# Optimization experiments

Hardware: AMD Instinct MI355X
Metric: run time of the kernel (lower is better)

Reference implementation:

```python
import jax, jax.numpy as jnp
import numpy as np

N_NODES = 10000
N_EDGES = 80000
IN_DIM = 1024
HID = 4096
OUT = 256


def sage_conv(x, src, dst, W_l, b_l, W_r, num_nodes):
    # mean aggregation of source-node features onto target nodes
    msg = x[src]                                            # [E, D] gather
    agg = jax.ops.segment_sum(msg, dst, num_segments=num_nodes)   # [N, D]
    cnt = jax.ops.segment_sum(jnp.ones((src.shape[0],), x.dtype), dst,
                              num_segments=num_nodes)       # [N]
    mean = agg / jnp.clip(cnt, 1.0)[:, None]                # isolated nodes -> 0
    # lin_l(mean) + lin_r(x); lin_r has no bias in PyG SAGEConv
    return mean @ W_l.T + b_l + x @ W_r.T


def setup_inputs() -> dict:
    key = jax.random.key(0)
    ks = jax.random.split(key, 6)
    x = jax.random.normal(ks[0], (N_NODES, IN_DIM), dtype=jnp.float32)
    edge_index = jax.random.randint(ks[1], (2, N_EDGES), 0, N_NODES, dtype=jnp.int32)
    s1 = 1.0 / np.sqrt(IN_DIM)
    s2 = 1.0 / np.sqrt(HID)
    W1_l = jax.random.normal(ks[2], (HID, IN_DIM), dtype=jnp.float32) * s1
    b1_l = jnp.zeros((HID,), jnp.float32)
    W1_r = jax.random.normal(ks[3], (HID, IN_DIM), dtype=jnp.float32) * s1
    W2_l = jax.random.normal(ks[4], (OUT, HID), dtype=jnp.float32) * s2
    b2_l = jnp.zeros((OUT,), jnp.float32)
    W2_r = jax.random.normal(ks[5], (OUT, HID), dtype=jnp.float32) * s2
    return {"x": x, "edge_index": edge_index, "W1_l": W1_l, "b1_l": b1_l,
            "W1_r": W1_r, "W2_l": W2_l, "b2_l": b2_l, "W2_r": W2_r}


def reference(x, edge_index, W1_l, b1_l, W1_r, W2_l, b2_l, W2_r):
    src, dst = edge_index[0], edge_index[1]
    h = sage_conv(x, src, dst, W1_l, b1_l, W1_r, N_NODES)   # [N, 4096]
    h = jax.nn.relu(h)
    # dropout is identity in eval mode
    out = sage_conv(h, src, dst, W2_l, b2_l, W2_r, N_NODES)  # [N, 256]
    return jax.nn.log_softmax(out, axis=1)
```

## Files before the change

### kernel.cpp

```cpp
#include <hip/hip_runtime.h>
#include <cstdint>
#include <cstddef>

#define DEVINL __device__ __forceinline__

typedef __bf16 bf16x8 __attribute__((ext_vector_type(8)));
typedef float f32x4 __attribute__((ext_vector_type(4)));

static constexpr int NN = 10000;
static constexpr int NE = 80000;
static constexpr int IN_DIM = 1024;
static constexpr int HID = 4096;
static constexpr int OUTD = 256;
static constexpr int M_PAD = 10112;

DEVINL unsigned short f2bf(float f) {
  unsigned int u = __builtin_bit_cast(unsigned int, f);
  u += 0x7fffu + ((u >> 16) & 1u);
  return (unsigned short)(u >> 16);
}

DEVINL void ld_lds16(const void* g, void* l) {
  __builtin_amdgcn_global_load_lds(
      (const __attribute__((address_space(1))) unsigned int*)g,
      (__attribute__((address_space(3))) unsigned int*)l, 16, 0, 0);
}

__global__ void deg_kernel(const int* __restrict__ dst, int* __restrict__ deg) {
  int e = blockIdx.x * 256 + threadIdx.x;
  if (e < NE) atomicAdd(&deg[dst[e]], 1);
}

__global__ __launch_bounds__(256) void scan_kernel(const int* __restrict__ deg,
                                                   int* __restrict__ offs) {
  __shared__ int part[256];
  constexpr int NPT = 40;
  int t = threadIdx.x;
  int base = t * NPT;
  int s = 0;
  for (int j = 0; j < NPT; ++j) {
    int n = base + j;
    s += (n < NN) ? deg[n] : 0;
  }
  part[t] = s;
  __syncthreads();
  for (int o = 1; o < 256; o <<= 1) {
    int v = (t >= o) ? part[t - o] : 0;
    __syncthreads();
    part[t] += v;
    __syncthreads();
  }
  int pre = (t > 0) ? part[t - 1] : 0;
  for (int j = 0; j < NPT; ++j) {
    int n = base + j;
    if (n < NN) {
      offs[n] = pre;
      pre += deg[n];
    }
  }
  if (t == 255) offs[NN] = part[255];
}

__global__ void bin_kernel(const int* __restrict__ src, const int* __restrict__ dst,
                           const int* __restrict__ offs, int* __restrict__ fill,
                           int* __restrict__ csr) {
  int e = blockIdx.x * 256 + threadIdx.x;
  if (e < NE) {
    int d = dst[e];
    int p = atomicAdd(&fill[d], 1);
    csr[offs[d] + p] = src[e];
  }
}

__global__ __launch_bounds__(256) void gather1_kernel(const float* __restrict__ x,
                                                      const int* __restrict__ offs,
                                                      const int* __restrict__ csr,
                                                      unsigned short* __restrict__ A1) {
  int i = blockIdx.x;
  int t = threadIdx.x;
  int beg = offs[i], end = offs[i + 1];
  float4 acc = {0.f, 0.f, 0.f, 0.f};
  for (int j = beg; j < end; ++j) {
    int s = __builtin_amdgcn_readfirstlane(csr[j]);
    float4 v = ((const float4*)(x + (size_t)s * IN_DIM))[t];
    acc.x += v.x; acc.y += v.y; acc.z += v.z; acc.w += v.w;
  }
  float inv = 1.0f / (float)max(end - beg, 1);
  float4 b = ((const float4*)(x + (size_t)i * IN_DIM))[t];
  ushort4 pa = {f2bf(acc.x * inv), f2bf(acc.y * inv), f2bf(acc.z * inv), f2bf(acc.w * inv)};
  ushort4 pb = {f2bf(b.x), f2bf(b.y), f2bf(b.z), f2bf(b.w)};
  unsigned short* row = A1 + (size_t)i * 2048;
  ((ushort4*)row)[t] = pa;
  ((ushort4*)(row + 1024))[t] = pb;
}

__global__ void conv_w1_kernel(const float* __restrict__ Wl, const float* __restrict__ Wr,
                               unsigned short* __restrict__ w1cat) {
  int g = blockIdx.x * 256 + threadIdx.x;
  int n = g >> 9;
  int kg = g & 511;
  const float* s = (kg < 256) ? (Wl + (size_t)n * 1024 + kg * 4)
                              : (Wr + (size_t)n * 1024 + (kg - 256) * 4);
  float4 v = *(const float4*)s;
  ushort4 p = {f2bf(v.x), f2bf(v.y), f2bf(v.z), f2bf(v.w)};
  ((ushort4*)w1cat)[g] = p;
}

__global__ void conv_w2_kernel(const float* __restrict__ Wl, const float* __restrict__ Wr,
                               unsigned short* __restrict__ w2cat) {
  int g = blockIdx.x * 256 + threadIdx.x;
  int n = g >> 10;
  int kg = g & 1023;
  const float* s = (n < 256) ? (Wl + (size_t)n * 4096 + kg * 4)
                             : (Wr + (size_t)(n - 256) * 4096 + kg * 4);
  float4 v = *(const float4*)s;
  ushort4 p = {f2bf(v.x), f2bf(v.y), f2bf(v.z), f2bf(v.w)};
  ((ushort4*)w2cat)[g] = p;
}

template <int BM, int K, int N, int NUMM, int NUMN, int GM, bool EPI_RELU_BF16>
__global__ __launch_bounds__(256) void gemm_kernel(const unsigned short* __restrict__ A,
                                                   const unsigned short* __restrict__ Bt,
                                                   const float* __restrict__ bias,
                                                   void* __restrict__ Cout) {
  constexpr int BN = 128;
  constexpr int MI = BM / 32;
  constexpr int NI = 4;
  constexpr int SA = BM / 64;
  constexpr int SB = BN / 64;
  __shared__ unsigned short Asm[BM * 32];
  __shared__ unsigned short Bsm[BN * 32];

  constexpr int NPG = GM * NUMN;
  const int pid = blockIdx.x;
  const int gid = pid / NPG;
  const int first_m = gid * GM;
  const int sz = (NUMM - first_m < GM) ? (NUMM - first_m) : GM;
  const int local = pid % NPG;
  const int pm = first_m + local % sz;
  const int pn = local / sz;

  const int tid = threadIdx.x;
  const int lane = tid & 63;
  const int wave = tid >> 6;
  const int quad = lane >> 4;
  const int l16 = lane & 15;
  const int wm = (wave & 1) * (BM / 2);
  const int wn = (wave >> 1) * 64;
  const long tm0 = (long)pm * BM;
  const long tn0 = (long)pn * BN;

  f32x4 acc[MI][NI];
#pragma unroll
  for (int i = 0; i < MI; ++i)
#pragma unroll
    for (int j = 0; j < NI; ++j) acc[i][j] = (f32x4){0.f, 0.f, 0.f, 0.f};

  const unsigned short* aSrc[SA];
  unsigned short* aDst[SA];
  const unsigned short* bSrc[SB];
  unsigned short* bDst[SB];
#pragma unroll
  for (int s = 0; s < SA; ++s) {
    int c = s * 256 + wave * 64 + lane;
    int r = c >> 2;
    int g = (c & 3) ^ ((r >> 1) & 3);
    aSrc[s] = A + (size_t)(tm0 + r) * K + g * 8;
    aDst[s] = Asm + s * 2048 + wave * 512;
  }
#pragma unroll
  for (int s = 0; s < SB; ++s) {
    int c = s * 256 + wave * 64 + lane;
    int r = c >> 2;
    int g = (c & 3) ^ ((r >> 1) & 3);
    bSrc[s] = Bt + (size_t)(tn0 + r) * K + g * 8;
    bDst[s] = Bsm + s * 2048 + wave * 512;
  }

  const int srd = quad ^ ((l16 >> 1) & 3);

  for (int k0 = 0; k0 < K; k0 += 32) {
#pragma unroll
    for (int s = 0; s < SA; ++s) ld_lds16(aSrc[s] + k0, aDst[s]);
#pragma unroll
    for (int s = 0; s < SB; ++s) ld_lds16(bSrc[s] + k0, bDst[s]);
    __syncthreads();

    bf16x8 af[MI], bv[NI];
#pragma unroll
    for (int i = 0; i < MI; ++i) {
      int ra = wm + i * 16 + l16;
      af[i] = *(const bf16x8*)(Asm + ra * 32 + srd * 8);
    }
#pragma unroll
    for (int j = 0; j < NI; ++j) {
      int rb = wn + j * 16 + l16;
      bv[j] = *(const bf16x8*)(Bsm + rb * 32 + srd * 8);
    }
#pragma unroll
    for (int i = 0; i < MI; ++i)
#pragma unroll
      for (int j = 0; j < NI; ++j)
        acc[i][j] = __builtin_amdgcn_mfma_f32_16x16x32_bf16(af[i], bv[j], acc[i][j], 0, 0, 0);
    __syncthreads();
  }

  if (EPI_RELU_BF16) {
    unsigned short* C = (unsigned short*)Cout;
#pragma unroll
    for (int i = 0; i < MI; ++i) {
      long m0 = tm0 + wm + i * 16 + quad * 4;
#pragma unroll
      for (int j = 0; j < NI; ++j) {
        int n = (int)tn0 + wn + j * 16 + l16;
        float bvs = bias[n];
#pragma unroll
        for (int r = 0; r < 4; ++r) {
          float v = acc[i][j][r] + bvs;
          v = fmaxf(v, 0.0f);
          C[(size_t)(m0 + r) * N + n] = f2bf(v);
        }
      }
    }
  } else {
    float* C = (float*)Cout;
#pragma unroll
    for (int i = 0; i < MI; ++i) {
      long m0 = tm0 + wm + i * 16 + quad * 4;
#pragma unroll
      for (int j = 0; j < NI; ++j) {
        int n = (int)tn0 + wn + j * 16 + l16;
#pragma unroll
        for (int r = 0; r < 4; ++r) C[(size_t)(m0 + r) * N + n] = acc[i][j][r];
      }
    }
  }
}

__global__ __launch_bounds__(256) void gather2_final_kernel(const float* __restrict__ C2,
                                                            const int* __restrict__ offs,
                                                            const int* __restrict__ csr,
                                                            const float* __restrict__ b2,
                                                            float* __restrict__ out) {
  int i = blockIdx.x;
  int t = threadIdx.x;
  int beg = offs[i], end = offs[i + 1];
  float acc = 0.f;
  for (int j = beg; j < end; ++j) {
    int s = __builtin_amdgcn_readfirstlane(csr[j]);
    acc += C2[(size_t)s * 512 + t];
  }
  float inv = 1.0f / (float)max(end - beg, 1);
  float v = acc * inv + b2[t] + C2[(size_t)i * 512 + 256 + t];

  __shared__ float sm[4], ss[4];
  int w = t >> 6;
  float m = v;
#pragma unroll
  for (int o = 32; o > 0; o >>= 1) m = fmaxf(m, __shfl_xor(m, o, 64));
  if ((t & 63) == 0) sm[w] = m;
  __syncthreads();
  m = fmaxf(fmaxf(sm[0], sm[1]), fmaxf(sm[2], sm[3]));

  float e = __expf(v - m);
  float s = e;
#pragma unroll
  for (int o = 32; o > 0; o >>= 1) s += __shfl_xor(s, o, 64);
  if ((t & 63) == 0) ss[w] = s;
  __syncthreads();
  s = ss[0] + ss[1] + ss[2] + ss[3];

  out[(size_t)i * OUTD + t] = v - m - logf(s);
}

static constexpr size_t OFF_A1 = 0;
static constexpr size_t OFF_W1 = OFF_A1 + (size_t)M_PAD * 2048 * 2;
static constexpr size_t OFF_HB = OFF_W1 + (size_t)HID * 2048 * 2;
static constexpr size_t OFF_W2 = OFF_HB + (size_t)M_PAD * HID * 2;
static constexpr size_t OFF_DEG = OFF_W2 + (size_t)512 * HID * 2;
static constexpr size_t OFF_OFFS = OFF_DEG + (size_t)NN * 4;
static constexpr size_t OFF_FILL = OFF_OFFS + (size_t)(NN + 4) * 4;
static constexpr size_t OFF_CSR = OFF_FILL + (size_t)NN * 4;

extern "C" void kernel_launch(void* const* d_in, const int* in_sizes, int n_in,
                              void* d_out, int out_size, void* d_ws, size_t ws_size,
                              hipStream_t stream) {
  const float* x = (const float*)d_in[0];
  const int* ei = (const int*)d_in[1];
  const int* src = ei;
  const int* dst = ei + NE;
  const float* W1_l = (const float*)d_in[2];
  const float* b1_l = (const float*)d_in[3];
  const float* W1_r = (const float*)d_in[4];
  const float* W2_l = (const float*)d_in[5];
  const float* b2_l = (const float*)d_in[6];
  const float* W2_r = (const float*)d_in[7];
  float* out = (float*)d_out;

  char* ws = (char*)d_ws;
  unsigned short* A1 = (unsigned short*)(ws + OFF_A1);
  unsigned short* w1cat = (unsigned short*)(ws + OFF_W1);
  unsigned short* h_b = (unsigned short*)(ws + OFF_HB);
  unsigned short* w2cat = (unsigned short*)(ws + OFF_W2);
  int* deg = (int*)(ws + OFF_DEG);
  int* offs = (int*)(ws + OFF_OFFS);
  int* fill = (int*)(ws + OFF_FILL);
  int* csr = (int*)(ws + OFF_CSR);
  float* C2 = (float*)(ws + OFF_A1);

  hipMemsetAsync(deg, 0, (size_t)NN * 4, stream);
  hipMemsetAsync(fill, 0, (size_t)NN * 4, stream);
  hipMemsetAsync(A1 + (size_t)NN * 2048, 0, (size_t)(M_PAD - NN) * 2048 * 2, stream);

  deg_kernel<<<(NE + 255) / 256, 256, 0, stream>>>(dst, deg);
  scan_kernel<<<1, 256, 0, stream>>>(deg, offs);
  bin_kernel<<<(NE + 255) / 256, 256, 0, stream>>>(src, dst, offs, fill, csr);

  conv_w1_kernel<<<(HID * 512) / 256, 256, 0, stream>>>(W1_l, W1_r, w1cat);
  conv_w2_kernel<<<(512 * 1024) / 256, 256, 0, stream>>>(W2_l, W2_r, w2cat);

  gather1_kernel<<<NN, 256, 0, stream>>>(x, offs, csr, A1);

  gemm_kernel<128, 2048, 4096, 79, 32, 32, true>
      <<<79 * 32, 256, 0, stream>>>(A1, w1cat, b1_l, h_b);
  gemm_kernel<64, 4096, 512, 158, 4, 64, false>
      <<<158 * 4, 256, 0, stream>>>(h_b, w2cat, nullptr, C2);

  gather2_final_kernel<<<NN, 256, 0, stream>>>(C2, offs, csr, b2_l, out);
}
```

Baseline: 514.0 us.

## Gather from bf16 copies of x and layer-2 partials; fuse prep kernels

Converts x to bf16 once in a merged prep kernel that also handles both weight conversions and the degree count, so the layer-1 gather reads half the bytes per neighbour. The layer-2 GEMM now writes the neighbour-aggregated half as bf16 and the self half as fp32 in separate buffers, and the final gather/log-softmax uses 128 threads that each handle two outputs. This cuts gather memory traffic and launch count, at the cost of summing bf16-rounded values rather than fp32 ones.

```diff
diff --git a/kernel.cpp b/kernel.cpp
--- a/kernel.cpp
+++ b/kernel.cpp
@@ -19,6 +19,10 @@
   u += 0x7fffu + ((u >> 16) & 1u);
   return (unsigned short)(u >> 16);
 }
+DEVINL float bf2f(unsigned short h) {
+  unsigned int u = ((unsigned int)h) << 16;
+  return __builtin_bit_cast(float, u);
+}
 
 DEVINL void ld_lds16(const void* g, void* l) {
   __builtin_amdgcn_global_load_lds(
@@ -26,9 +30,48 @@
       (__attribute__((address_space(3))) unsigned int*)l, 16, 0, 0);
 }
 
-__global__ void deg_kernel(const int* __restrict__ dst, int* __restrict__ deg) {
-  int e = blockIdx.x * 256 + threadIdx.x;
-  if (e < NE) atomicAdd(&deg[dst[e]], 1);
+static constexpr int PREP_B1 = 8192;
+static constexpr int PREP_B2 = PREP_B1 + 2048;
+static constexpr int PREP_B3 = PREP_B2 + 10000;
+static constexpr int PREP_NB = PREP_B3 + 313;
+
+__global__ __launch_bounds__(256) void prep_kernel(
+    const float* __restrict__ W1l, const float* __restrict__ W1r,
+    const float* __restrict__ W2l, const float* __restrict__ W2r,
+    const float* __restrict__ x, const int* __restrict__ dst,
+    unsigned short* __restrict__ w1cat, unsigned short* __restrict__ w2cat,
+    unsigned short* __restrict__ x_bf, int* __restrict__ deg) {
+  int b = blockIdx.x;
+  int t = threadIdx.x;
+  if (b < PREP_B1) {
+    int g = b * 256 + t;
+    int n = g >> 9;
+    int kg = g & 511;
+    const float* s = (kg < 256) ? (W1l + (size_t)n * 1024 + kg * 4)
+                                : (W1r + (size_t)n * 1024 + (kg - 256) * 4);
+    float4 v = *(const float4*)s;
+    ushort4 p = {f2bf(v.x), f2bf(v.y), f2bf(v.z), f2bf(v.w)};
+    ((ushort4*)w1cat)[g] = p;
+  } else if (b < PREP_B2) {
+    int g = (b - PREP_B1) * 256 + t;
+    int n = g >> 10;
+    int kg = g & 1023;
+    const float* s = (n < 256) ? (W2l + (size_t)n * 4096 + kg * 4)
+                               : (W2r + (size_t)(n - 256) * 4096 + kg * 4);
+    float4 v = *(const float4*)s;
+    ushort4 p = {f2bf(v.x), f2bf(v.y), f2bf(v.z), f2bf(v.w)};
+    ((ushort4*)w2cat)[g] = p;
+  } else if (b < PREP_B3) {
+    int g = (b - PREP_B2) * 256 + t;
+    int i = g >> 8;
+    int kg = g & 255;
+    float4 v = ((const float4*)(x + (size_t)i * IN_DIM))[kg];
+    ushort4 p = {f2bf(v.x), f2bf(v.y), f2bf(v.z), f2bf(v.w)};
+    ((ushort4*)(x_bf + (size_t)i * IN_DIM))[kg] = p;
+  } else {
+    int e = (b - PREP_B3) * 256 + t;
+    if (e < NE) atomicAdd(&deg[dst[e]], 1);
+  }
 }
 
 __global__ __launch_bounds__(256) void scan_kernel(const int* __restrict__ deg,
@@ -72,7 +115,7 @@
   }
 }
 
-__global__ __launch_bounds__(256) void gather1_kernel(const float* __restrict__ x,
+__global__ __launch_bounds__(256) void gather1_kernel(const unsigned short* __restrict__ x_bf,
                                                       const int* __restrict__ offs,
                                                       const int* __restrict__ csr,
                                                       unsigned short* __restrict__ A1) {
@@ -82,47 +125,23 @@
   float4 acc = {0.f, 0.f, 0.f, 0.f};
   for (int j = beg; j < end; ++j) {
     int s = __builtin_amdgcn_readfirstlane(csr[j]);
-    float4 v = ((const float4*)(x + (size_t)s * IN_DIM))[t];
-    acc.x += v.x; acc.y += v.y; acc.z += v.z; acc.w += v.w;
+    ushort4 u = ((const ushort4*)(x_bf + (size_t)s * IN_DIM))[t];
+    acc.x += bf2f(u.x); acc.y += bf2f(u.y); acc.z += bf2f(u.z); acc.w += bf2f(u.w);
   }
   float inv = 1.0f / (float)max(end - beg, 1);
-  float4 b = ((const float4*)(x + (size_t)i * IN_DIM))[t];
+  ushort4 ub = ((const ushort4*)(x_bf + (size_t)i * IN_DIM))[t];
   ushort4 pa = {f2bf(acc.x * inv), f2bf(acc.y * inv), f2bf(acc.z * inv), f2bf(acc.w * inv)};
-  ushort4 pb = {f2bf(b.x), f2bf(b.y), f2bf(b.z), f2bf(b.w)};
   unsigned short* row = A1 + (size_t)i * 2048;
   ((ushort4*)row)[t] = pa;
-  ((ushort4*)(row + 1024))[t] = pb;
-}
-
-__global__ void conv_w1_kernel(const float* __restrict__ Wl, const float* __restrict__ Wr,
-                               unsigned short* __restrict__ w1cat) {
-  int g = blockIdx.x * 256 + threadIdx.x;
-  int n = g >> 9;
-  int kg = g & 511;
-  const float* s = (kg < 256) ? (Wl + (size_t)n * 1024 + kg * 4)
-                              : (Wr + (size_t)n * 1024 + (kg - 256) * 4);
-  float4 v = *(const float4*)s;
-  ushort4 p = {f2bf(v.x), f2bf(v.y), f2bf(v.z), f2bf(v.w)};
-  ((ushort4*)w1cat)[g] = p;
-}
-
-__global__ void conv_w2_kernel(const float* __restrict__ Wl, const float* __restrict__ Wr,
-                               unsigned short* __restrict__ w2cat) {
-  int g = blockIdx.x * 256 + threadIdx.x;
-  int n = g >> 10;
-  int kg = g & 1023;
-  const float* s = (n < 256) ? (Wl + (size_t)n * 4096 + kg * 4)
-                             : (Wr + (size_t)(n - 256) * 4096 + kg * 4);
-  float4 v = *(const float4*)s;
-  ushort4 p = {f2bf(v.x), f2bf(v.y), f2bf(v.z), f2bf(v.w)};
-  ((ushort4*)w2cat)[g] = p;
-}
-
-template <int BM, int K, int N, int NUMM, int NUMN, int GM, bool EPI_RELU_BF16>
+  ((ushort4*)(row + 1024))[t] = ub;
+}
+
+template <int BM, int K, int N, int NUMM, int NUMN, int GM, int EPI>
 __global__ __launch_bounds__(256) void gemm_kernel(const unsigned short* __restrict__ A,
                                                    const unsigned short* __restrict__ Bt,
                                                    const float* __restrict__ bias,
-                                                   void* __restrict__ Cout) {
+                                                   void* __restrict__ C0out,
+                                                   void* __restrict__ C1out) {
   constexpr int BN = 128;
   constexpr int MI = BM / 32;
   constexpr int NI = 4;
@@ -205,8 +224,8 @@
     __syncthreads();
   }
 
-  if (EPI_RELU_BF16) {
-    unsigned short* C = (unsigned short*)Cout;
+  if (EPI == 1) {
+    unsigned short* C = (unsigned short*)C0out;
 #pragma unroll
     for (int i = 0; i < MI; ++i) {
       long m0 = tm0 + wm + i * 16 + quad * 4;
@@ -223,21 +242,28 @@
       }
     }
   } else {
-    float* C = (float*)Cout;
+    unsigned short* PL = (unsigned short*)C0out;
+    float* PR = (float*)C1out;
 #pragma unroll
     for (int i = 0; i < MI; ++i) {
       long m0 = tm0 + wm + i * 16 + quad * 4;
 #pragma unroll
       for (int j = 0; j < NI; ++j) {
         int n = (int)tn0 + wn + j * 16 + l16;
-#pragma unroll
-        for (int r = 0; r < 4; ++r) C[(size_t)(m0 + r) * N + n] = acc[i][j][r];
+        if (n < 256) {
+#pragma unroll
+          for (int r = 0; r < 4; ++r) PL[(size_t)(m0 + r) * 256 + n] = f2bf(acc[i][j][r]);
+        } else {
+#pragma unroll
+          for (int r = 0; r < 4; ++r) PR[(size_t)(m0 + r) * 256 + (n - 256)] = acc[i][j][r];
+        }
       }
     }
   }
 }
 
-__global__ __launch_bounds__(256) void gather2_final_kernel(const float* __restrict__ C2,
+__global__ __launch_bounds__(128) void gather2_final_kernel(const unsigned short* __restrict__ pl,
+                                                            const float* __restrict__ pr,
                                                             const int* __restrict__ offs,
                                                             const int* __restrict__ csr,
                                                             const float* __restrict__ b2,
@@ -245,42 +271,50 @@
   int i = blockIdx.x;
   int t = threadIdx.x;
   int beg = offs[i], end = offs[i + 1];
-  float acc = 0.f;
+  float a0 = 0.f, a1 = 0.f;
   for (int j = beg; j < end; ++j) {
     int s = __builtin_amdgcn_readfirstlane(csr[j]);
-    acc += C2[(size_t)s * 512 + t];
+    unsigned int u = ((const unsigned int*)(pl + (size_t)s * 256))[t];
+    a0 += bf2f((unsigned short)(u & 0xffffu));
+    a1 += bf2f((unsigned short)(u >> 16));
   }
   float inv = 1.0f / (float)max(end - beg, 1);
-  float v = acc * inv + b2[t] + C2[(size_t)i * 512 + 256 + t];
-
-  __shared__ float sm[4], ss[4];
+  float2 bv = ((const float2*)b2)[t];
+  float2 pv = ((const float2*)(pr + (size_t)i * 256))[t];
+  float v0 = a0 * inv + bv.x + pv.x;
+  float v1 = a1 * inv + bv.y + pv.y;
+
+  __shared__ float sm[2], ss[2];
   int w = t >> 6;
-  float m = v;
+  float m = fmaxf(v0, v1);
 #pragma unroll
   for (int o = 32; o > 0; o >>= 1) m = fmaxf(m, __shfl_xor(m, o, 64));
   if ((t & 63) == 0) sm[w] = m;
   __syncthreads();
-  m = fmaxf(fmaxf(sm[0], sm[1]), fmaxf(sm[2], sm[3]));
-
-  float e = __expf(v - m);
-  float s = e;
+  m = fmaxf(sm[0], sm[1]);
+
+  float s = __expf(v0 - m) + __expf(v1 - m);
 #pragma unroll
   for (int o = 32; o > 0; o >>= 1) s += __shfl_xor(s, o, 64);
   if ((t & 63) == 0) ss[w] = s;
   __syncthreads();
-  s = ss[0] + ss[1] + ss[2] + ss[3];
-
-  out[(size_t)i * OUTD + t] = v - m - logf(s);
+  float ls = logf(ss[0] + ss[1]);
+
+  float2 o2 = {v0 - m - ls, v1 - m - ls};
+  ((float2*)(out + (size_t)i * OUTD))[t] = o2;
 }
 
 static constexpr size_t OFF_A1 = 0;
 static constexpr size_t OFF_W1 = OFF_A1 + (size_t)M_PAD * 2048 * 2;
 static constexpr size_t OFF_HB = OFF_W1 + (size_t)HID * 2048 * 2;
 static constexpr size_t OFF_W2 = OFF_HB + (size_t)M_PAD * HID * 2;
+static constexpr size_t OFF_XBF = OFF_W2 - (size_t)NN * IN_DIM * 2;
 static constexpr size_t OFF_DEG = OFF_W2 + (size_t)512 * HID * 2;
 static constexpr size_t OFF_OFFS = OFF_DEG + (size_t)NN * 4;
 static constexpr size_t OFF_FILL = OFF_OFFS + (size_t)(NN + 4) * 4;
 static constexpr size_t OFF_CSR = OFF_FILL + (size_t)NN * 4;
+static constexpr size_t OFF_PL = OFF_A1;
+static constexpr size_t OFF_PR = OFF_PL + (size_t)M_PAD * 256 * 2;
 
 extern "C" void kernel_launch(void* const* d_in, const int* in_sizes, int n_in,
                               void* d_out, int out_size, void* d_ws, size_t ws_size,
@@ -301,30 +335,30 @@
   unsigned short* A1 = (unsigned short*)(ws + OFF_A1);
   unsigned short* w1cat = (unsigned short*)(ws + OFF_W1);
   unsigned short* h_b = (unsigned short*)(ws + OFF_HB);
+  unsigned short* x_bf = (unsigned short*)(ws + OFF_XBF);
   unsigned short* w2cat = (unsigned short*)(ws + OFF_W2);
   int* deg = (int*)(ws + OFF_DEG);
   int* offs = (int*)(ws + OFF_OFFS);
   int* fill = (int*)(ws + OFF_FILL);
   int* csr = (int*)(ws + OFF_CSR);
-  float* C2 = (float*)(ws + OFF_A1);
+  unsigned short* pl = (unsigned short*)(ws + OFF_PL);
+  float* pr = (float*)(ws + OFF_PR);
 
   hipMemsetAsync(deg, 0, (size_t)NN * 4, stream);
   hipMemsetAsync(fill, 0, (size_t)NN * 4, stream);
   hipMemsetAsync(A1 + (size_t)NN * 2048, 0, (size_t)(M_PAD - NN) * 2048 * 2, stream);
 
-  deg_kernel<<<(NE + 255) / 256, 256, 0, stream>>>(dst, deg);
+  prep_kernel<<<PREP_NB, 256, 0, stream>>>(W1_l, W1_r, W2_l, W2_r, x, dst,
+                                           w1cat, w2cat, x_bf, deg);
   scan_kernel<<<1, 256, 0, stream>>>(deg, offs);
   bin_kernel<<<(NE + 255) / 256, 256, 0, stream>>>(src, dst, offs, fill, csr);
 
-  conv_w1_kernel<<<(HID * 512) / 256, 256, 0, stream>>>(W1_l, W1_r, w1cat);
-  conv_w2_kernel<<<(512 * 1024) / 256, 256, 0, stream>>>(W2_l, W2_r, w2cat);
-
-  gather1_kernel<<<NN, 256, 0, stream>>>(x, offs, csr, A1);
-
-  gemm_kernel<128, 2048, 4096, 79, 32, 32, true>
-      <<<79 * 32, 256, 0, stream>>>(A1, w1cat, b1_l, h_b);
-  gemm_kernel<64, 4096, 512, 158, 4, 64, false>
-      <<<158 * 4, 256, 0, stream>>>(h_b, w2cat, nullptr, C2);
-
-  gather2_final_kernel<<<NN, 256, 0, stream>>>(C2, offs, csr, b2_l, out);
-}
+  gather1_kernel<<<NN, 256, 0, stream>>>(x_bf, offs, csr, A1);
+
+  gemm_kernel<128, 2048, 4096, 79, 32, 32, 1>
+      <<<79 * 32, 256, 0, stream>>>(A1, w1cat, b1_l, h_b, nullptr);
+  gemm_kernel<64, 4096, 512, 158, 4, 64, 2>
+      <<<158 * 4, 256, 0, stream>>>(h_b, w2cat, nullptr, pl, pr);
+
+  gather2_final_kernel<<<NN, 128, 0, stream>>>(pl, pr, offs, csr, b2_l, out);
+}
```

Result: faster. 483.9 us (-5.9%).
